# Optimization experiments

Measured on AMD Instinct MI355X. Metric: run time of the kernel, lower is better.

## Reference

```python
import jax, jax.numpy as jnp
import numpy as np

B, C, N = 2, 32, 4096
EPS = 1e-5


def _batchnorm1d(x, gamma, bias):
    # BatchNorm1d in training mode: stats over (batch, spatial) per channel, biased var
    mean = x.mean(axis=(0, 2), keepdims=True)
    var = x.var(axis=(0, 2), keepdims=True)
    return (x - mean) * jax.lax.rsqrt(var + EPS) * gamma[None, :, None] + bias[None, :, None]


def setup_inputs() -> dict:
    key = jax.random.key(0)
    k1, k2, k3 = jax.random.split(key, 3)
    Feature = jax.random.normal(k1, (B, C, N), dtype=jnp.float32)
    gamma = jnp.ones((C,), dtype=jnp.float32)
    bn_bias = jnp.zeros((C,), dtype=jnp.float32)
    alpha = jax.random.uniform(k2, (), dtype=jnp.float32)
    beta = jax.random.uniform(k3, (), dtype=jnp.float32)
    return {"Feature": Feature, "gamma": gamma, "bn_bias": bn_bias, "alpha": alpha, "beta": beta}


def reference(Feature, gamma, bn_bias, alpha, beta):
    a = Feature                                   # [B, C, N]
    # --- PAM: BN + ReLU prologue, then spatial N x N attention ---
    f = jax.nn.relu(_batchnorm1d(Feature, gamma, bn_bias))
    cb = jnp.einsum('bcn,bcm->bnm', f, f)         # c^T c : [B, N, N]
    s = jax.nn.softmax(cb, axis=1)                # softmax over dim=1 (as in source)
    e_p = jnp.einsum('bcn,bmn->bcm', f, s)        # c @ s^T : [B, C, N]
    pam = alpha * e_p + a
    # --- CAM: channel C x C attention, softmax over batch axis (dim=0 as in source) ---
    aa = jnp.einsum('bcn,bdn->bdc', a, a)         # matmul(a, a^T).permute(0,2,1) : [B, C, C]
    x = jax.nn.softmax(aa, axis=0)
    e_c = jnp.einsum('bji,bjn->bin', x, a)        # x^T @ a : [B, C, N]
    cam = beta * e_c + a
    return pam + cam
```

## Files before the change

### kernel.cpp

```cpp
#include <hip/hip_runtime.h>
#include <math.h>


#define BB 2
#define CC 32
#define NN 4096
#define EPSV 1e-5f
#define SQL2E 1.2011224087864498f

typedef short short8 __attribute__((ext_vector_type(8)));
typedef float f32x4 __attribute__((ext_vector_type(4)));

#define OFF_FNC  0
#define OFF_FCN  131072
#define OFF_M    262144
#define OFF_XW   270336
#define OFF_AAP  272384
#define OFF_S1P  305152
#define OFF_S2P  305408
#define OFF_Z    305664

__device__ inline ushort f2bf(float x) {
    uint u = __float_as_uint(x);
    uint r = u + 0x7FFFu + ((u >> 16) & 1u);
    return (ushort)(r >> 16);
}
__device__ inline float bf2f(ushort h) { return __uint_as_float(((uint)h) << 16); }
__device__ inline uint packbf(float lo, float hi) {
    return (__float_as_uint(hi) & 0xFFFF0000u) | (__float_as_uint(lo) >> 16);
}

__global__ void __launch_bounds__(256) k_pre(const float* __restrict__ x,
                                             float* __restrict__ ws) {
    __shared__ float smem[4352];
    const int blk = blockIdx.x, t = threadIdx.x;
    const int lane = t & 63, wv = t >> 6;
    if (blk < 256) {
        const int c = blk & 31, chunk = blk >> 5;
        const int i0 = chunk * 1024;
        const int b = i0 >> 12, n0 = i0 & (NN - 1);
        const float4 v = *(const float4*)(x + ((size_t)(b * CC + c)) * NN + n0 + t * 4);
        float s  = v.x + v.y + v.z + v.w;
        float s2 = v.x * v.x + v.y * v.y + v.z * v.z + v.w * v.w;
        for (int off = 32; off; off >>= 1) { s += __shfl_down(s, off); s2 += __shfl_down(s2, off); }
        if (lane == 0) { smem[wv] = s; smem[4 + wv] = s2; }
        __syncthreads();
        if (t == 0) {
            ws[OFF_S1P + chunk * 32 + c] = smem[0] + smem[1] + smem[2] + smem[3];
            ws[OFF_S2P + chunk * 32 + c] = smem[4] + smem[5] + smem[6] + smem[7];
        }
    } else {
        const int blk2 = blk - 256;
        const int b = blk2 >> 4, chnk = blk2 & 15;
        const int nb = chnk * 256;
        const int d = t >> 3, cg4 = (t & 7) * 4;
        float a0 = 0.f, a1 = 0.f, a2 = 0.f, a3 = 0.f;
        for (int it = 0; it < 2; ++it) {
            __syncthreads();
            for (int li = t; li < 4096; li += 256) {
                const int row = li >> 7, col = li & 127;
                smem[row * 132 + col] = x[((size_t)(b * CC + row)) * NN + nb + it * 128 + col];
            }
            __syncthreads();
            for (int k = 0; k < 128; ++k) {
                const float vd = smem[d * 132 + k];
                a0 += smem[(cg4 + 0) * 132 + k] * vd;
                a1 += smem[(cg4 + 1) * 132 + k] * vd;
                a2 += smem[(cg4 + 2) * 132 + k] * vd;
                a3 += smem[(cg4 + 3) * 132 + k] * vd;
            }
        }
        float* dst = ws + OFF_AAP + ((size_t)((b * 16 + chnk) * CC + d)) * CC + cg4;
        dst[0] = a0; dst[1] = a1; dst[2] = a2; dst[3] = a3;
    }
}

__global__ void __launch_bounds__(256) k_makef(const float* __restrict__ x,
                                               const float* __restrict__ gamma,
                                               const float* __restrict__ bias,
                                               float* __restrict__ ws) {
    __shared__ float ssc[CC], ssh[CC];
    __shared__ ushort tS[CC][18];
    const int blk = blockIdx.x, t = threadIdx.x;
    const int base = blk * 16;
    const int b = base >> 12, n0 = base & (NN - 1);
    if (t < CC) {
        float S1 = 0.f, S2 = 0.f;
        #pragma unroll
        for (int k = 0; k < 8; ++k) { S1 += ws[OFF_S1P + k * 32 + t]; S2 += ws[OFF_S2P + k * 32 + t]; }
        const float mean = S1 * (1.f / (BB * NN));
        const float var = S2 * (1.f / (BB * NN)) - mean * mean;
        const float sc = gamma[t] * rsqrtf(var + EPSV);
        ssc[t] = sc; ssh[t] = bias[t] - mean * sc;
    }
    __syncthreads();
    {
        const int c = t >> 3, cp = t & 7;
        const float2 v = *(const float2*)(x + ((size_t)(b * CC + c)) * NN + n0 + 2 * cp);
        const float f0 = fmaxf(v.x * ssc[c] + ssh[c], 0.f);
        const float f1 = fmaxf(v.y * ssc[c] + ssh[c], 0.f);
        const ushort h0u = f2bf(f0), h1u = f2bf(f1);
        ((uint*)((ushort*)(ws + OFF_FCN) + ((size_t)(b * CC + c)) * NN + n0))[cp] =
            (uint)h0u | ((uint)h1u << 16);
        const ushort h0s = f2bf(f0 * SQL2E), h1s = f2bf(f1 * SQL2E);
        tS[c][2 * cp]     = h0s;
        tS[c][2 * cp + 1] = h1s;
    }
    __syncthreads();
    if (t < 64) {
        const int col = t >> 2, q = t & 3;
        union { ushort us[8]; short8 v; } r;
        #pragma unroll
        for (int j = 0; j < 8; ++j) r.us[j] = tS[q * 8 + j][col];
        *(short8*)((ushort*)(ws + OFF_FNC) + ((size_t)(base + col)) * CC + q * 8) = r.v;
    } else if (t < 80) {
        const int col = t - 64;
        float msum = 0.f;
        #pragma unroll
        for (int c = 0; c < CC; ++c) { const float fs = bf2f(tS[c][col]); msum += fs * fs; }
        ws[OFF_M + base + col] = msum;
    } else if (t < 96) {
        ws[OFF_Z + blk * 16 + (t - 80)] = 0.f;
    }
}

__global__ void __launch_bounds__(256) k_zpass(float* __restrict__ ws) {
    const int blk = blockIdx.x, t = threadIdx.x;
    if (blk == 2048) {
        for (int li = t; li < CC * CC; li += 256) {
            const int i = li >> 5, j = li & 31;
            float q0 = 0.f, q1 = 0.f;
            for (int cchunk = 0; cchunk < 16; ++cchunk) {
                q0 += ws[OFF_AAP + ((size_t)((0 * 16 + cchunk) * CC + j)) * CC + i];
                q1 += ws[OFF_AAP + ((size_t)((1 * 16 + cchunk) * CC + j)) * CC + i];
            }
            const float mx = fmaxf(q0, q1);
            const float e0 = __expf(q0 - mx), e1 = __expf(q1 - mx);
            const float inv = 1.f / (e0 + e1);
            ws[OFF_XW + 0 * 1024 + i * 32 + j] = e0 * inv;
            ws[OFF_XW + 1 * 1024 + i * 32 + j] = e1 * inv;
        }
        return;
    }
    const ushort* fnc = (const ushort*)(ws + OFF_FNC);
    const int lane = t & 63, wv = t >> 6;
    const int ml = lane & 15, kg = lane >> 4;
    const f32x4 fzero = {0.f, 0.f, 0.f, 0.f};
    const int b = blk >> 10;
    const int rem = blk & 1023;
    const int ng = rem >> 5;
    const int mch = rem & 31;
    const int nbA = ng * 128 + wv * 16, nbB = nbA + 64;
    const short8 bfA = *(const short8*)(fnc + ((size_t)(b * NN + nbA + ml)) * CC + kg * 8);
    const short8 bfB = *(const short8*)(fnc + ((size_t)(b * NN + nbB + ml)) * CC + kg * 8);
    const float MA = ws[OFF_M + b * NN + nbA + ml];
    const float MB = ws[OFF_M + b * NN + nbB + ml];
    float zA = 0.f, zB = 0.f;
    const int m0 = mch * 128;
    for (int mm = m0; mm < m0 + 128; mm += 16) {
        const short8 af = *(const short8*)(fnc + ((size_t)(b * NN + mm + ml)) * CC + kg * 8);
        f32x4 dA = __builtin_amdgcn_mfma_f32_16x16x32_bf16(af, bfA, fzero, 0, 0, 0);
        f32x4 dB = __builtin_amdgcn_mfma_f32_16x16x32_bf16(af, bfB, fzero, 0, 0, 0);
        zA += exp2f(dA[0] - MA) + exp2f(dA[1] - MA) + exp2f(dA[2] - MA) + exp2f(dA[3] - MA);
        zB += exp2f(dB[0] - MB) + exp2f(dB[1] - MB) + exp2f(dB[2] - MB) + exp2f(dB[3] - MB);
    }
    zA += __shfl_xor(zA, 16); zA += __shfl_xor(zA, 32);
    zB += __shfl_xor(zB, 16); zB += __shfl_xor(zB, 32);
    if (lane < 16) {
        atomicAdd(ws + OFF_Z + b * NN + nbA + ml, zA);
        atomicAdd(ws + OFF_Z + b * NN + nbB + ml, zB);
    }
}

__global__ void __launch_bounds__(512) k_epfinal(const float* __restrict__ x,
                                                 const float* __restrict__ alpha_p,
                                                 const float* __restrict__ beta_p,
                                                 const float* __restrict__ ws,
                                                 float* __restrict__ out) {
    __shared__ float red[8][512];
    __shared__ float sM[NN];
    __shared__ float sZi[NN];
    __shared__ float sxw[CC * 33];
    __shared__ float sa[CC * 16];
    const ushort* fnc = (const ushort*)(ws + OFF_FNC);
    const ushort* fcn = (const ushort*)(ws + OFF_FCN);
    const int blk = blockIdx.x, t = threadIdx.x;
    const int lane = t & 63, wv = t >> 6;
    const int ml = lane & 15, kg = lane >> 4;
    const f32x4 fzero = {0.f, 0.f, 0.f, 0.f};
    const int b = blk >> 8, mg = blk & 255;
    const int mb = mg * 16;

    {
        const float* Mp = ws + OFF_M + b * NN;
        const float* Zp = ws + OFF_Z + b * NN;
        #pragma unroll
        for (int i = t; i < NN / 4; i += 512) {
            const float4 z = *(const float4*)(Zp + i * 4);
            const float4 m = *(const float4*)(Mp + i * 4);
            ((float4*)sZi)[i] = make_float4(__builtin_amdgcn_rcpf(z.x), __builtin_amdgcn_rcpf(z.y),
                                            __builtin_amdgcn_rcpf(z.z), __builtin_amdgcn_rcpf(z.w));
            ((float4*)sM)[i] = m;
        }
        const int j = t >> 4, mcol = t & 15;
        sa[j * 16 + mcol] = x[((size_t)(b * CC + j)) * NN + mb + mcol];
        for (int li = t; li < CC * CC; li += 512)
            sxw[(li >> 5) * 33 + (li & 31)] = ws[OFF_XW + b * 1024 + li];
    }
    __syncthreads();

    const short8 bm = *(const short8*)(fnc + ((size_t)(b * NN + mb + ml)) * CC + kg * 8);
    f32x4 acc0 = fzero, acc1 = fzero;
    const int n0beg = wv * 512;
    for (int n0 = n0beg; n0 < n0beg + 512; n0 += 32) {
        const short8 an0 = *(const short8*)(fnc + ((size_t)(b * NN + n0      + ml)) * CC + kg * 8);
        const short8 an1 = *(const short8*)(fnc + ((size_t)(b * NN + n0 + 16 + ml)) * CC + kg * 8);
        f32x4 d0 = __builtin_amdgcn_mfma_f32_16x16x32_bf16(an0, bm, fzero, 0, 0, 0);
        f32x4 d1 = __builtin_amdgcn_mfma_f32_16x16x32_bf16(an1, bm, fzero, 0, 0, 0);
        const float4 M0 = *(const float4*)(sM + n0 + kg * 4);
        const float4 M1 = *(const float4*)(sM + n0 + 16 + kg * 4);
        const float4 Z0 = *(const float4*)(sZi + n0 + kg * 4);
        const float4 Z1 = *(const float4*)(sZi + n0 + 16 + kg * 4);
        const float w00 = exp2f(d0[0] - M0.x) * Z0.x;
        const float w01 = exp2f(d0[1] - M0.y) * Z0.y;
        const float w02 = exp2f(d0[2] - M0.z) * Z0.z;
        const float w03 = exp2f(d0[3] - M0.w) * Z0.w;
        const float w10 = exp2f(d1[0] - M1.x) * Z1.x;
        const float w11 = exp2f(d1[1] - M1.y) * Z1.y;
        const float w12 = exp2f(d1[2] - M1.z) * Z1.z;
        const float w13 = exp2f(d1[3] - M1.w) * Z1.w;
        const uint p0 = packbf(w00, w01), p1 = packbf(w02, w03);
        const uint q0 = packbf(w10, w11), q1 = packbf(w12, w13);
        union { uint u[4]; short8 s; } wf;
        {
            const int s0 = (((kg & 1) << 1) + 0) * 16 + ml;
            const int s1 = (((kg & 1) << 1) + 1) * 16 + ml;
            const uint vp0 = __shfl(p0, s0), vp1 = __shfl(p1, s0);
            const uint vp2 = __shfl(p0, s1), vp3 = __shfl(p1, s1);
            const uint vq0 = __shfl(q0, s0), vq1 = __shfl(q1, s0);
            const uint vq2 = __shfl(q0, s1), vq3 = __shfl(q1, s1);
            const bool hi = (kg >= 2);
            wf.u[0] = hi ? vq0 : vp0; wf.u[1] = hi ? vq1 : vp1;
            wf.u[2] = hi ? vq2 : vp2; wf.u[3] = hi ? vq3 : vp3;
        }
        const short8 a20 = *(const short8*)(fcn + ((size_t)(b * CC + ml))      * NN + n0 + kg * 8);
        const short8 a21 = *(const short8*)(fcn + ((size_t)(b * CC + 16 + ml)) * NN + n0 + kg * 8);
        acc0 = __builtin_amdgcn_mfma_f32_16x16x32_bf16(a20, wf.s, acc0, 0, 0, 0);
        acc1 = __builtin_amdgcn_mfma_f32_16x16x32_bf16(a21, wf.s, acc1, 0, 0, 0);
    }
    #pragma unroll
    for (int r = 0; r < 4; ++r) {
        red[wv][(kg * 4 + r) * 16 + ml]      = acc0[r];
        red[wv][(16 + kg * 4 + r) * 16 + ml] = acc1[r];
    }
    __syncthreads();
    float ep = 0.f;
    #pragma unroll
    for (int w = 0; w < 8; ++w) ep += red[w][t];
    const float alpha = *alpha_p, beta = *beta_p;
    const int c = t >> 4, m2 = t & 15;
    float ec = 0.f;
    #pragma unroll
    for (int j = 0; j < CC; ++j) ec += sxw[c * 33 + j] * sa[j * 16 + m2];
    const float av = sa[c * 16 + m2];
    out[((size_t)(b * CC + c)) * NN + mb + m2] = alpha * ep + beta * ec + 2.f * av;
}

extern "C" void kernel_launch(void* const* d_in, const int* in_sizes, int n_in,
                              void* d_out, int out_size, void* d_ws, size_t ws_size,
                              hipStream_t stream) {
    const float* x     = (const float*)d_in[0];
    const float* gamma = (const float*)d_in[1];
    const float* bias  = (const float*)d_in[2];
    const float* alpha = (const float*)d_in[3];
    const float* beta  = (const float*)d_in[4];
    float* out = (float*)d_out;
    float* ws  = (float*)d_ws;

    hipLaunchKernelGGL(k_pre,     dim3(288),  dim3(256), 0, stream, x, ws);
    hipLaunchKernelGGL(k_makef,   dim3(512),  dim3(256), 0, stream, x, gamma, bias, ws);
    hipLaunchKernelGGL(k_zpass,   dim3(2049), dim3(256), 0, stream, ws);
    hipLaunchKernelGGL(k_epfinal, dim3(512),  dim3(512), 0, stream, x, alpha, beta, ws, out);
}
```

Before: 124.8 us.

## Fuse BN feature build into softmax-denominator pass and halve CAM partial chunks

Merges the BN+ReLU feature-building kernel into the softmax denominator kernel. Each block rebuilds its bf16 n and m tiles in LDS directly from x, and only the mch==0 blocks write the features out to the workspace for the final kernel. This removes one launch and the global round trip for the A/B fragments, at the cost of redundantly recomputing normalized tiles from x in each of the 16 m-chunks. The channel Gram partials are split into 32 chunks of 128 instead of 16 chunks of 256 for more parallelism, and Z zeroing moves into k_pre.

```diff
diff --git a/kernel.cpp b/kernel.cpp
--- a/kernel.cpp
+++ b/kernel.cpp
@@ -16,9 +16,9 @@
 #define OFF_M    262144
 #define OFF_XW   270336
 #define OFF_AAP  272384
-#define OFF_S1P  305152
-#define OFF_S2P  305408
-#define OFF_Z    305664
+#define OFF_S1P  337920
+#define OFF_S2P  338176
+#define OFF_Z    338432
 
 __device__ inline ushort f2bf(float x) {
     uint u = __float_as_uint(x);
@@ -32,10 +32,10 @@
 
 __global__ void __launch_bounds__(256) k_pre(const float* __restrict__ x,
                                              float* __restrict__ ws) {
-    __shared__ float smem[4352];
+    __shared__ float smem[4224];
     const int blk = blockIdx.x, t = threadIdx.x;
-    const int lane = t & 63, wv = t >> 6;
     if (blk < 256) {
+        const int lane = t & 63, wv = t >> 6;
         const int c = blk & 31, chunk = blk >> 5;
         const int i0 = chunk * 1024;
         const int b = i0 >> 12, n0 = i0 & (NN - 1);
@@ -44,6 +44,7 @@
         float s2 = v.x * v.x + v.y * v.y + v.z * v.z + v.w * v.w;
         for (int off = 32; off; off >>= 1) { s += __shfl_down(s, off); s2 += __shfl_down(s2, off); }
         if (lane == 0) { smem[wv] = s; smem[4 + wv] = s2; }
+        if (t < 32) ws[OFF_Z + blk * 32 + t] = 0.f;
         __syncthreads();
         if (t == 0) {
             ws[OFF_S1P + chunk * 32 + c] = smem[0] + smem[1] + smem[2] + smem[3];
@@ -51,88 +52,39 @@
         }
     } else {
         const int blk2 = blk - 256;
-        const int b = blk2 >> 4, chnk = blk2 & 15;
-        const int nb = chnk * 256;
+        const int b = blk2 >> 5, chnk = blk2 & 31;
+        const int nb = chnk * 128;
+        for (int li = t; li < 4096; li += 256) {
+            const int row = li >> 7, col = li & 127;
+            smem[row * 132 + col] = x[((size_t)(b * CC + row)) * NN + nb + col];
+        }
+        __syncthreads();
         const int d = t >> 3, cg4 = (t & 7) * 4;
         float a0 = 0.f, a1 = 0.f, a2 = 0.f, a3 = 0.f;
-        for (int it = 0; it < 2; ++it) {
-            __syncthreads();
-            for (int li = t; li < 4096; li += 256) {
-                const int row = li >> 7, col = li & 127;
-                smem[row * 132 + col] = x[((size_t)(b * CC + row)) * NN + nb + it * 128 + col];
-            }
-            __syncthreads();
-            for (int k = 0; k < 128; ++k) {
-                const float vd = smem[d * 132 + k];
-                a0 += smem[(cg4 + 0) * 132 + k] * vd;
-                a1 += smem[(cg4 + 1) * 132 + k] * vd;
-                a2 += smem[(cg4 + 2) * 132 + k] * vd;
-                a3 += smem[(cg4 + 3) * 132 + k] * vd;
-            }
-        }
-        float* dst = ws + OFF_AAP + ((size_t)((b * 16 + chnk) * CC + d)) * CC + cg4;
+        for (int k = 0; k < 128; ++k) {
+            const float vd = smem[d * 132 + k];
+            a0 += smem[(cg4 + 0) * 132 + k] * vd;
+            a1 += smem[(cg4 + 1) * 132 + k] * vd;
+            a2 += smem[(cg4 + 2) * 132 + k] * vd;
+            a3 += smem[(cg4 + 3) * 132 + k] * vd;
+        }
+        float* dst = ws + OFF_AAP + ((size_t)((b * 32 + chnk) * CC + d)) * CC + cg4;
         dst[0] = a0; dst[1] = a1; dst[2] = a2; dst[3] = a3;
     }
 }
 
-__global__ void __launch_bounds__(256) k_makef(const float* __restrict__ x,
+__global__ void __launch_bounds__(256) k_zmake(const float* __restrict__ x,
                                                const float* __restrict__ gamma,
                                                const float* __restrict__ bias,
                                                float* __restrict__ ws) {
-    __shared__ float ssc[CC], ssh[CC];
-    __shared__ ushort tS[CC][18];
     const int blk = blockIdx.x, t = threadIdx.x;
-    const int base = blk * 16;
-    const int b = base >> 12, n0 = base & (NN - 1);
-    if (t < CC) {
-        float S1 = 0.f, S2 = 0.f;
-        #pragma unroll
-        for (int k = 0; k < 8; ++k) { S1 += ws[OFF_S1P + k * 32 + t]; S2 += ws[OFF_S2P + k * 32 + t]; }
-        const float mean = S1 * (1.f / (BB * NN));
-        const float var = S2 * (1.f / (BB * NN)) - mean * mean;
-        const float sc = gamma[t] * rsqrtf(var + EPSV);
-        ssc[t] = sc; ssh[t] = bias[t] - mean * sc;
-    }
-    __syncthreads();
-    {
-        const int c = t >> 3, cp = t & 7;
-        const float2 v = *(const float2*)(x + ((size_t)(b * CC + c)) * NN + n0 + 2 * cp);
-        const float f0 = fmaxf(v.x * ssc[c] + ssh[c], 0.f);
-        const float f1 = fmaxf(v.y * ssc[c] + ssh[c], 0.f);
-        const ushort h0u = f2bf(f0), h1u = f2bf(f1);
-        ((uint*)((ushort*)(ws + OFF_FCN) + ((size_t)(b * CC + c)) * NN + n0))[cp] =
-            (uint)h0u | ((uint)h1u << 16);
-        const ushort h0s = f2bf(f0 * SQL2E), h1s = f2bf(f1 * SQL2E);
-        tS[c][2 * cp]     = h0s;
-        tS[c][2 * cp + 1] = h1s;
-    }
-    __syncthreads();
-    if (t < 64) {
-        const int col = t >> 2, q = t & 3;
-        union { ushort us[8]; short8 v; } r;
-        #pragma unroll
-        for (int j = 0; j < 8; ++j) r.us[j] = tS[q * 8 + j][col];
-        *(short8*)((ushort*)(ws + OFF_FNC) + ((size_t)(base + col)) * CC + q * 8) = r.v;
-    } else if (t < 80) {
-        const int col = t - 64;
-        float msum = 0.f;
-        #pragma unroll
-        for (int c = 0; c < CC; ++c) { const float fs = bf2f(tS[c][col]); msum += fs * fs; }
-        ws[OFF_M + base + col] = msum;
-    } else if (t < 96) {
-        ws[OFF_Z + blk * 16 + (t - 80)] = 0.f;
-    }
-}
-
-__global__ void __launch_bounds__(256) k_zpass(float* __restrict__ ws) {
-    const int blk = blockIdx.x, t = threadIdx.x;
-    if (blk == 2048) {
+    if (blk == 1024) {
         for (int li = t; li < CC * CC; li += 256) {
             const int i = li >> 5, j = li & 31;
             float q0 = 0.f, q1 = 0.f;
-            for (int cchunk = 0; cchunk < 16; ++cchunk) {
-                q0 += ws[OFF_AAP + ((size_t)((0 * 16 + cchunk) * CC + j)) * CC + i];
-                q1 += ws[OFF_AAP + ((size_t)((1 * 16 + cchunk) * CC + j)) * CC + i];
+            for (int ch = 0; ch < 32; ++ch) {
+                q0 += ws[OFF_AAP + ((size_t)((0 * 32 + ch) * CC + j)) * CC + i];
+                q1 += ws[OFF_AAP + ((size_t)((1 * 32 + ch) * CC + j)) * CC + i];
             }
             const float mx = fmaxf(q0, q1);
             const float e0 = __expf(q0 - mx), e1 = __expf(q1 - mx);
@@ -142,23 +94,68 @@
         }
         return;
     }
-    const ushort* fnc = (const ushort*)(ws + OFF_FNC);
+    __shared__ ushort tileA[256 * 40];
+    __shared__ ushort tileB[128 * 40];
+    __shared__ float ssc[CC], ssh[CC], sMloc[128];
+    const int b = blk >> 9;
+    const int rem = blk & 511;
+    const int ng = rem >> 4, mch = rem & 15;
+    const int nb = ng * 128, m0 = mch * 256;
+    const bool writer = (mch == 0);
+    if (t < CC) {
+        float S1 = 0.f, S2 = 0.f;
+        #pragma unroll
+        for (int k = 0; k < 8; ++k) { S1 += ws[OFF_S1P + k * 32 + t]; S2 += ws[OFF_S2P + k * 32 + t]; }
+        const float mean = S1 * (1.f / (BB * NN));
+        const float var = S2 * (1.f / (BB * NN)) - mean * mean;
+        const float sc = gamma[t] * rsqrtf(var + EPSV);
+        ssc[t] = sc; ssh[t] = bias[t] - mean * sc;
+    }
+    __syncthreads();
+    #pragma unroll
+    for (int i = 0; i < 16; ++i) {
+        const int li = i * 256 + t;
+        const int c = li >> 7, n1 = li & 127;
+        const float v = x[((size_t)(b * CC + c)) * NN + nb + n1];
+        const float f = fmaxf(v * ssc[c] + ssh[c], 0.f);
+        if (writer) ((ushort*)(ws + OFF_FCN))[((size_t)(b * CC + c)) * NN + nb + n1] = f2bf(f);
+        tileB[n1 * 40 + c] = f2bf(f * SQL2E);
+    }
+    #pragma unroll
+    for (int i = 0; i < 32; ++i) {
+        const int li = i * 256 + t;
+        const int c = li >> 8, m1 = li & 255;
+        const float v = x[((size_t)(b * CC + c)) * NN + m0 + m1];
+        const float f = fmaxf(v * ssc[c] + ssh[c], 0.f);
+        tileA[m1 * 40 + c] = f2bf(f * SQL2E);
+    }
+    __syncthreads();
+    if (t < 128) {
+        union { ushort us[8]; short8 v8; } r[4];
+        #pragma unroll
+        for (int q = 0; q < 4; ++q) r[q].v8 = *(const short8*)(tileB + t * 40 + q * 8);
+        float ms = 0.f;
+        #pragma unroll
+        for (int j = 0; j < 32; ++j) { const float fv = bf2f(r[j >> 3].us[j & 7]); ms += fv * fv; }
+        sMloc[t] = ms;
+        if (writer) {
+            ws[OFF_M + b * NN + nb + t] = ms;
+            ushort* dst = (ushort*)(ws + OFF_FNC) + ((size_t)(b * NN + nb + t)) * CC;
+            #pragma unroll
+            for (int q = 0; q < 4; ++q) *(short8*)(dst + q * 8) = r[q].v8;
+        }
+    }
+    __syncthreads();
     const int lane = t & 63, wv = t >> 6;
     const int ml = lane & 15, kg = lane >> 4;
     const f32x4 fzero = {0.f, 0.f, 0.f, 0.f};
-    const int b = blk >> 10;
-    const int rem = blk & 1023;
-    const int ng = rem >> 5;
-    const int mch = rem & 31;
-    const int nbA = ng * 128 + wv * 16, nbB = nbA + 64;
-    const short8 bfA = *(const short8*)(fnc + ((size_t)(b * NN + nbA + ml)) * CC + kg * 8);
-    const short8 bfB = *(const short8*)(fnc + ((size_t)(b * NN + nbB + ml)) * CC + kg * 8);
-    const float MA = ws[OFF_M + b * NN + nbA + ml];
-    const float MB = ws[OFF_M + b * NN + nbB + ml];
+    const short8 bfA = *(const short8*)(tileB + (wv * 16 + ml) * 40 + kg * 8);
+    const short8 bfB = *(const short8*)(tileB + (wv * 16 + 64 + ml) * 40 + kg * 8);
+    const float MA = sMloc[wv * 16 + ml];
+    const float MB = sMloc[wv * 16 + 64 + ml];
     float zA = 0.f, zB = 0.f;
-    const int m0 = mch * 128;
-    for (int mm = m0; mm < m0 + 128; mm += 16) {
-        const short8 af = *(const short8*)(fnc + ((size_t)(b * NN + mm + ml)) * CC + kg * 8);
+    for (int mm = 0; mm < 256; mm += 16) {
+        const short8 af = *(const short8*)(tileA + (mm + ml) * 40 + kg * 8);
         f32x4 dA = __builtin_amdgcn_mfma_f32_16x16x32_bf16(af, bfA, fzero, 0, 0, 0);
         f32x4 dB = __builtin_amdgcn_mfma_f32_16x16x32_bf16(af, bfB, fzero, 0, 0, 0);
         zA += exp2f(dA[0] - MA) + exp2f(dA[1] - MA) + exp2f(dA[2] - MA) + exp2f(dA[3] - MA);
@@ -167,8 +164,8 @@
     zA += __shfl_xor(zA, 16); zA += __shfl_xor(zA, 32);
     zB += __shfl_xor(zB, 16); zB += __shfl_xor(zB, 32);
     if (lane < 16) {
-        atomicAdd(ws + OFF_Z + b * NN + nbA + ml, zA);
-        atomicAdd(ws + OFF_Z + b * NN + nbB + ml, zB);
+        atomicAdd(ws + OFF_Z + b * NN + nb + wv * 16 + ml, zA);
+        atomicAdd(ws + OFF_Z + b * NN + nb + wv * 16 + 64 + ml, zB);
     }
 }
 
@@ -277,8 +274,7 @@
     float* out = (float*)d_out;
     float* ws  = (float*)d_ws;
 
-    hipLaunchKernelGGL(k_pre,     dim3(288),  dim3(256), 0, stream, x, ws);
-    hipLaunchKernelGGL(k_makef,   dim3(512),  dim3(256), 0, stream, x, gamma, bias, ws);
-    hipLaunchKernelGGL(k_zpass,   dim3(2049), dim3(256), 0, stream, ws);
+    hipLaunchKernelGGL(k_pre,     dim3(320),  dim3(256), 0, stream, x, ws);
+    hipLaunchKernelGGL(k_zmake,   dim3(1025), dim3(256), 0, stream, x, gamma, bias, ws);
     hipLaunchKernelGGL(k_epfinal, dim3(512),  dim3(512), 0, stream, x, alpha, beta, ws, out);
 }
```

Result: slower. 147.3 us (+18.0%).
